# Kernel tuning notes

Measured on AMD Instinct MI355X. Metric: run time of the kernel, lower is better.

Reference implementation:

```python
import jax, jax.numpy as jnp
import numpy as np

IGNORE = -100000.0


def setup_inputs() -> dict:
    key = jax.random.key(0)
    ks = jax.random.split(key, 5)
    b, s, d_model = 4, 2048, 2048
    n_q, n_kv, d_head = 32, 8, 64
    std = 0.02
    return {
        "normalized_resid_pre": jax.random.normal(ks[0], (b, s, d_model), jnp.float32),
        "W_Q": jax.random.normal(ks[1], (n_q, d_model, d_head), jnp.float32) * std,
        "W_K": jax.random.normal(ks[2], (n_kv, d_model, d_head), jnp.float32) * std,
        "W_V": jax.random.normal(ks[3], (n_kv, d_model, d_head), jnp.float32) * std,
        "W_O": jax.random.normal(ks[4], (n_kv, d_head, d_model), jnp.float32) * std,
    }


def reference(normalized_resid_pre, W_Q, W_K, W_V, W_O):
    x = normalized_resid_pre
    b, s, _ = x.shape
    n_kv, d_head = W_K.shape[0], W_K.shape[2]
    n_q = W_Q.shape[0]
    g = n_q // n_kv

    q = jnp.einsum("bpd,hdk->bphk", x, W_Q)  # [b,s,n_q,d_head]
    k = jnp.einsum("bpd,ndk->bpnk", x, W_K)  # [b,s,n_kv,d_head]
    v = jnp.einsum("bpd,ndk->bpnk", x, W_V)  # [b,s,n_kv,d_head]

    # rearrange: head axis splits as (n_kv_heads, g_size), then moved to [b,s,g,n_kv,d_head]
    gq = q.reshape(b, s, n_kv, g, d_head).transpose(0, 1, 3, 2, 4)

    # NOTE: faithful to source — g axis is SUMMED in this einsum
    scores = jnp.einsum("bqgnh,bknh->bnqk", gq, k) / jnp.sqrt(jnp.float32(d_head))

    causal = jnp.triu(jnp.ones((s, s), dtype=bool), k=1)  # True above diagonal
    scores = jnp.where(causal, IGNORE, scores)
    pattern = jax.nn.softmax(scores, axis=-1)  # [b,n_kv,q,k]

    z = jnp.einsum("bknh,bnqk->bqnh", v, pattern)  # [b,s,n_kv,d_head]
    attn_out = jnp.einsum("bqnh,nhd->bqd", z, W_O)  # [b,s,d_model]
    return attn_out
```

## Files before the change

### kernel.cpp

```cpp
#include <hip/hip_runtime.h>

typedef __attribute__((ext_vector_type(8))) _Float16 half8;
typedef __attribute__((ext_vector_type(4))) float f32x4;

#define BATCH  4
#define SLEN   2048
#define DMODEL 2048
#define NKV    8
#define GRP    4
#define DH     64
#define QKV    1536
#define KVDIM  512
#define MROWS  (BATCH * SLEN)

__device__ __forceinline__ unsigned short f2h(float f) {
    union { _Float16 h; unsigned short u; } cv;
    cv.h = (_Float16)f;
    return cv.u;
}

__device__ __forceinline__ void gl16(const void* g, void* l) {
    __builtin_amdgcn_global_load_lds(
        (const __attribute__((address_space(1))) void*)g,
        (__attribute__((address_space(3))) void*)l, 16, 0, 0);
}

typedef __attribute__((ext_vector_type(4))) short short4v;
union U64S4 { unsigned long long u; short4v s; };

__global__ __launch_bounds__(256) void k_pack(const float* __restrict__ wq,
                                              const float* __restrict__ wk,
                                              const float* __restrict__ wv,
                                              float* __restrict__ wcat) {
    int i = blockIdx.x * 256 + threadIdx.x;
    if (i >= DMODEL * QKV) return;
    int d = i / QKV, c = i - d * QKV;
    int mat = c >> 9, rem = c & 511;
    int n = rem >> 6, h = rem & 63;
    float val;
    if (mat == 0) {
        val = 0.0f;
#pragma unroll
        for (int g = 0; g < GRP; ++g)
            val += wq[((size_t)(n * GRP + g) * DMODEL + d) * DH + h];
    } else if (mat == 1) {
        val = wk[((size_t)n * DMODEL + d) * DH + h];
    } else {
        val = wv[((size_t)n * DMODEL + d) * DH + h];
    }
    wcat[(size_t)d * QKV + c] = val;
}

__global__ __launch_bounds__(256) void k_transconv_h(const float* __restrict__ in,
                                                     unsigned short* __restrict__ outT,
                                                     int R, int C) {
    __shared__ float T[64][65];
    const int r0 = blockIdx.x * 64, c0 = blockIdx.y * 64;
    const int tr = threadIdx.x >> 6, tc = threadIdx.x & 63;
#pragma unroll
    for (int i = 0; i < 16; ++i)
        T[tr + i * 4][tc] = in[(size_t)(r0 + tr + i * 4) * C + c0 + tc];
    __syncthreads();
    const int rr = tc;
#pragma unroll
    for (int i = 0; i < 16; ++i) {
        int cc = tr + i * 4;
        outT[(size_t)(c0 + cc) * R + r0 + rr] = f2h(T[rr][cc]);
    }
}

__global__ __launch_bounds__(256) void k_convh(const float* __restrict__ in,
                                               unsigned short* __restrict__ out,
                                               int n4) {
    int i = blockIdx.x * 256 + threadIdx.x;
    if (i >= n4) return;
    float4 v = ((const float4*)in)[i];
    ushort4 o;
    o.x = f2h(v.x); o.y = f2h(v.y); o.z = f2h(v.z); o.w = f2h(v.w);
    ((ushort4*)out)[i] = o;
}

__device__ __forceinline__ void stage_tile64(const unsigned short* __restrict__ src,
                                             unsigned short* lds, int t, int K, int k0) {
#pragma unroll
    for (int j = 0; j < 4; ++j) {
        int slot = j * 256 + t;
        int row = slot >> 3, blk = slot & 7;
        int c = blk ^ (row & 7);
        gl16(src + (size_t)row * K + k0 + c * 8, lds + slot * 8);
    }
}

#define GEMMF16_MAIN(Ag, Bg, K_)                                              \
    const int t = threadIdx.x;                                                \
    const size_t m0 = (size_t)blockIdx.x * 128, n0 = (size_t)blockIdx.y * 128;\
    const int w = t >> 6, l = t & 63;                                         \
    const int wm = (w >> 1) * 64, wn = (w & 1) * 64;                          \
    const int r = l & 15, q = l >> 4;                                         \
    f32x4 acc[4][4] = {};                                                     \
    const int K = (K_);                                                       \
    const int NT = K / 64;                                                    \
    stage_tile64(Ag + m0 * K, A2[0], t, K, 0);                                \
    stage_tile64(Bg + n0 * K, B2[0], t, K, 0);                                \
    asm volatile("s_waitcnt vmcnt(0)" ::: "memory");                          \
    __builtin_amdgcn_s_barrier();                                             \
    int cur = 0;                                                              \
    for (int kt = 0; kt < NT; ++kt) {                                         \
        if (kt + 1 < NT) {                                                    \
            stage_tile64(Ag + m0 * K, A2[cur ^ 1], t, K, (kt + 1) * 64);      \
            stage_tile64(Bg + n0 * K, B2[cur ^ 1], t, K, (kt + 1) * 64);      \
        }                                                                     \
        const unsigned short* Ac = A2[cur];                                   \
        const unsigned short* Bc = B2[cur];                                   \
        half8 af[4][2], bf[4][2];                                             \
        _Pragma("unroll") for (int i = 0; i < 4; ++i)                         \
            _Pragma("unroll") for (int ks = 0; ks < 2; ++ks) {                \
                int ra = wm + i * 16 + r;                                     \
                af[i][ks] = *(const half8*)&Ac[ra * 64 +                      \
                    ((((ks << 2) | q) ^ (ra & 7)) << 3)];                     \
                int rb = wn + i * 16 + r;                                     \
                bf[i][ks] = *(const half8*)&Bc[rb * 64 +                      \
                    ((((ks << 2) | q) ^ (rb & 7)) << 3)];                     \
            }                                                                 \
        __builtin_amdgcn_s_setprio(1);                                        \
        _Pragma("unroll") for (int i = 0; i < 4; ++i)                         \
            _Pragma("unroll") for (int j = 0; j < 4; ++j) {                   \
                acc[i][j] = __builtin_amdgcn_mfma_f32_16x16x32_f16(           \
                    af[i][0], bf[j][0], acc[i][j], 0, 0, 0);                  \
                acc[i][j] = __builtin_amdgcn_mfma_f32_16x16x32_f16(           \
                    af[i][1], bf[j][1], acc[i][j], 0, 0, 0);                  \
            }                                                                 \
        __builtin_amdgcn_s_setprio(0);                                        \
        asm volatile("s_waitcnt vmcnt(0)" ::: "memory");                      \
        __builtin_amdgcn_s_barrier();                                         \
        cur ^= 1;                                                             \
    }

__global__ __launch_bounds__(256) void k_gemm_qkv(
        const unsigned short* __restrict__ Ag, const unsigned short* __restrict__ Bg,
        unsigned short* __restrict__ qk, unsigned short* __restrict__ vT) {
    __shared__ unsigned short A2[2][128 * 64];
    __shared__ unsigned short B2[2][128 * 64];

    GEMMF16_MAIN(Ag, Bg, DMODEL)

    if (n0 < 1024) {
#pragma unroll
        for (int i = 0; i < 4; ++i)
#pragma unroll
            for (int j = 0; j < 4; ++j) {
                int col = (int)n0 + wn + j * 16 + r;
                size_t rowb = m0 + wm + i * 16 + q * 4;
#pragma unroll
                for (int e = 0; e < 4; ++e)
                    qk[(rowb + e) * 1024 + col] = f2h(acc[i][j][e]);
            }
    } else {
#pragma unroll
        for (int i = 0; i < 4; ++i)
#pragma unroll
            for (int j = 0; j < 4; ++j) {
                int d = (int)n0 - 1024 + wn + j * 16 + r;
                size_t rowb = m0 + wm + i * 16 + q * 4;
                ushort4 pk;
                pk.x = f2h(acc[i][j][0]); pk.y = f2h(acc[i][j][1]);
                pk.z = f2h(acc[i][j][2]); pk.w = f2h(acc[i][j][3]);
                *(ushort4*)&vT[(size_t)d * MROWS + rowb] = pk;
            }
    }
}

__global__ __launch_bounds__(256) void k_gemm_out(
        const unsigned short* __restrict__ Ag, const unsigned short* __restrict__ Bg,
        float* __restrict__ C) {
    __shared__ unsigned short A2[2][128 * 64];
    __shared__ unsigned short B2[2][128 * 64];

    GEMMF16_MAIN(Ag, Bg, KVDIM)

#pragma unroll
    for (int i = 0; i < 4; ++i)
#pragma unroll
        for (int j = 0; j < 4; ++j) {
            int col = (int)n0 + wn + j * 16 + r;
            size_t rowb = m0 + wm + i * 16 + q * 4;
#pragma unroll
            for (int e = 0; e < 4; ++e)
                C[(rowb + e) * DMODEL + col] = acc[i][j][e];
        }
}

__global__ __launch_bounds__(256) void k_attn_mfma(
        const unsigned short* __restrict__ qk, const unsigned short* __restrict__ vT,
        unsigned short* __restrict__ zh) {
    __shared__ unsigned short Ks[2][128 * 64];
    __shared__ unsigned short Vs[2][64 * 128];
    __shared__ unsigned short Pt[4 * 128 * 16];

    const int t  = threadIdx.x;
    const int w  = t >> 6, l = t & 63;
    const int p  = blockIdx.x;
    const int n  = blockIdx.y, b = blockIdx.z;
    const int r  = l & 15, g = l >> 4;
    const int wq0 = w * 16;

#define STAGE_KV(buf, kr0)                                                    \
    _Pragma("unroll") for (int j2 = 0; j2 < 4; ++j2) {                        \
        int s2 = j2 * 256 + t;                                                \
        int rK = s2 >> 3, cK = (s2 & 7) ^ (rK & 7);                           \
        gl16(qk + ((kr0) + rK) * 1024 + 512 + n * 64 + cK * 8,                \
             &Ks[buf][s2 * 8]);                                               \
        int rV = s2 >> 4, cV = (s2 & 15) ^ (rV & 15);                         \
        gl16(vT + (size_t)(n * 64 + rV) * MROWS + (kr0) + cV * 8,             \
             &Vs[buf][s2 * 8]);                                               \
    }

#pragma unroll 1
    for (int seg = 0; seg < 2; ++seg) {
        const int qt = seg ? p : (31 - p);
        const int nkt = (qt + 2) >> 1;
        const size_t qrow0 = (size_t)(b * SLEN + qt * 64);

        half8 qh[2];
#pragma unroll
        for (int ks = 0; ks < 2; ++ks) {
            size_t off = (qrow0 + wq0 + r) * 1024 + n * 64 + ks * 32 + g * 8;
            qh[ks] = *(const half8*)(qk + off);
#pragma unroll
            for (int e2 = 0; e2 < 8; ++e2) qh[ks][e2] = qh[ks][e2] * (_Float16)0.125f;
        }

        STAGE_KV(0, (size_t)(b * SLEN))
        asm volatile("s_waitcnt vmcnt(0)" ::: "memory");
        __builtin_amdgcn_s_barrier();

        float m_[4], lsum[4];
#pragma unroll
        for (int e = 0; e < 4; ++e) { m_[e] = -3.0e38f; lsum[e] = 0.0f; }
        f32x4 accz[4] = {};

        for (int kt = 0; kt < nkt; ++kt) {
            const int cur = kt & 1;
            if (kt + 1 < nkt) {
                STAGE_KV(cur ^ 1, (size_t)(b * SLEN + (kt + 1) * 128))
            }
            const unsigned short* Ksc = Ks[cur];
            const unsigned short* Vsc = Vs[cur];

            f32x4 s[8] = {};
#pragma unroll
            for (int ct = 0; ct < 8; ++ct)
#pragma unroll
                for (int ks = 0; ks < 2; ++ks) {
                    int row = ct * 16 + r;
                    int off = row * 128 + (((ks * 4 + g) ^ (row & 7)) << 4);
                    half8 kh8 = *(const half8*)((char*)Ksc + off);
                    s[ct] = __builtin_amdgcn_mfma_f32_16x16x32_f16(qh[ks], kh8, s[ct], 0, 0, 0);
                }

            if (kt == nkt - 1) {
#pragma unroll
                for (int ct = 0; ct < 8; ++ct)
#pragma unroll
                    for (int e = 0; e < 4; ++e)
                        if ((kt * 128 + ct * 16 + r) > (qt * 64 + wq0 + g * 4 + e))
                            s[ct][e] = -100000.0f;
            }

            float al[4], nm[4];
#pragma unroll
            for (int e = 0; e < 4; ++e) {
                float pm = fmaxf(fmaxf(fmaxf(s[0][e], s[1][e]), fmaxf(s[2][e], s[3][e])),
                                 fmaxf(fmaxf(s[4][e], s[5][e]), fmaxf(s[6][e], s[7][e])));
                pm = fmaxf(pm, __shfl_xor(pm, 1));
                pm = fmaxf(pm, __shfl_xor(pm, 2));
                pm = fmaxf(pm, __shfl_xor(pm, 4));
                pm = fmaxf(pm, __shfl_xor(pm, 8));
                nm[e] = fmaxf(m_[e], pm);
                al[e] = __expf(m_[e] - nm[e]);
                m_[e] = nm[e];
            }
            {
                int src = (r >> 2) << 4;
                float a0 = __shfl(al[0], src), a1 = __shfl(al[1], src);
                float a2 = __shfl(al[2], src), a3 = __shfl(al[3], src);
                float ax = (r & 1) ? a1 : a0, ay = (r & 1) ? a3 : a2;
                float aq = (r & 2) ? ay : ax;
#pragma unroll
                for (int dt = 0; dt < 4; ++dt) {
                    accz[dt][0] *= aq; accz[dt][1] *= aq;
                    accz[dt][2] *= aq; accz[dt][3] *= aq;
                }
            }

            float ps[4] = {};
#pragma unroll
            for (int ct = 0; ct < 8; ++ct) {
                float p0 = __expf(s[ct][0] - m_[0]);
                float p1 = __expf(s[ct][1] - m_[1]);
                float p2 = __expf(s[ct][2] - m_[2]);
                float p3 = __expf(s[ct][3] - m_[3]);
                ps[0] += p0; ps[1] += p1; ps[2] += p2; ps[3] += p3;
                short4v pk = { (short)f2h(p0), (short)f2h(p1),
                               (short)f2h(p2), (short)f2h(p3) };
                int kv = ct * 16 + r;
                int phys = (kv >> 5) * 32 + (((kv >> 2) & 1) << 4)
                         + (((kv >> 3) & 3) << 2) + (kv & 3);
                *(short4v*)((char*)Pt + w * 4096 + phys * 32 + g * 8) = pk;
            }

#pragma unroll
            for (int e = 0; e < 4; ++e) {
                float rs = ps[e];
                rs += __shfl_xor(rs, 1); rs += __shfl_xor(rs, 2);
                rs += __shfl_xor(rs, 4); rs += __shfl_xor(rs, 8);
                lsum[e] = lsum[e] * al[e] + rs;
            }

            asm volatile("s_waitcnt lgkmcnt(0)" ::: "memory");
            __builtin_amdgcn_sched_barrier(0);
#pragma unroll
            for (int ks = 0; ks < 4; ++ks) {
                unsigned base = (unsigned)(size_t)((char*)Pt + w * 4096 + ks * 1024) + l * 8;
                U64S4 t1, t2;
                asm volatile("ds_read_b64_tr_b16 %0, %1" : "=v"(t1.u) : "v"(base) : "memory");
                asm volatile("ds_read_b64_tr_b16 %0, %1" : "=v"(t2.u) : "v"(base + 512) : "memory");
                asm volatile("s_waitcnt lgkmcnt(0)" ::: "memory");
                __builtin_amdgcn_sched_barrier(0);
                short4v pa = t1.s, pb = t2.s;
                union { short s[8]; half8 h; } pf;
                pf.s[0] = pa[0]; pf.s[1] = pa[1]; pf.s[2] = pa[2]; pf.s[3] = pa[3];
                pf.s[4] = pb[0]; pf.s[5] = pb[1]; pf.s[6] = pb[2]; pf.s[7] = pb[3];
#pragma unroll
                for (int dt = 0; dt < 4; ++dt) {
                    int d = dt * 16 + r;
                    int off = d * 256 + (((ks * 4 + g) ^ (d & 15)) << 4);
                    half8 vfrag = *(const half8*)((char*)Vsc + off);
                    accz[dt] = __builtin_amdgcn_mfma_f32_16x16x32_f16(vfrag, pf.h, accz[dt], 0, 0, 0);
                }
            }

            asm volatile("s_waitcnt vmcnt(0)" ::: "memory");
            __builtin_amdgcn_s_barrier();
        }

        int src = (r >> 2) << 4;
        float l0 = __shfl(lsum[0], src), l1 = __shfl(lsum[1], src);
        float l2 = __shfl(lsum[2], src), l3 = __shfl(lsum[3], src);
        float lx = (r & 1) ? l1 : l0, ly = (r & 1) ? l3 : l2;
        float inv = 1.0f / ((r & 2) ? ly : lx);
#pragma unroll
        for (int dt = 0; dt < 4; ++dt) {
            ushort4 h4;
#pragma unroll
            for (int e = 0; e < 4; ++e)
                ((unsigned short*)&h4)[e] = f2h(accz[dt][e] * inv);
            size_t off = (qrow0 + wq0 + r) * 512 + n * 64 + dt * 16 + g * 4;
            *(ushort4*)(zh + off) = h4;
        }
    }
#undef STAGE_KV
}

extern "C" void kernel_launch(void* const* d_in, const int* in_sizes, int n_in,
                              void* d_out, int out_size, void* d_ws, size_t ws_size,
                              hipStream_t stream) {
    const float* x  = (const float*)d_in[0];
    const float* wq = (const float*)d_in[1];
    const float* wk = (const float*)d_in[2];
    const float* wv = (const float*)d_in[3];
    const float* wo = (const float*)d_in[4];
    float* out = (float*)d_out;

    char* w = (char*)d_ws;
    unsigned short* xh  = (unsigned short*)(w);
    unsigned short* zh  = (unsigned short*)(w);
    unsigned short* qk  = (unsigned short*)(w + 33554432);
    unsigned short* vT  = (unsigned short*)(w + 50331648);
    unsigned short* wcatT = (unsigned short*)(w + 58720256);
    unsigned short* woT = (unsigned short*)(w + 65011712);
    float*          wcat = (float*)(w + 67108864);

    k_pack<<<dim3((DMODEL * QKV + 255) / 256), 256, 0, stream>>>(wq, wk, wv, wcat);
    k_transconv_h<<<dim3(32, 24), 256, 0, stream>>>(wcat, wcatT, DMODEL, QKV);
    k_transconv_h<<<dim3(8, 32), 256, 0, stream>>>(wo, woT, KVDIM, DMODEL);
    k_convh<<<dim3(16384), 256, 0, stream>>>(x, xh, MROWS * DMODEL / 4);
    k_gemm_qkv<<<dim3(64, 12), 256, 0, stream>>>(xh, wcatT, qk, vT);
    k_attn_mfma<<<dim3(16, NKV, BATCH), 256, 0, stream>>>(qk, vT, zh);
    k_gemm_out<<<dim3(64, 16), 256, 0, stream>>>(zh, woT, out);
}
```

Measured before the change: 201.4 us.

## Fuse weight pack with transpose-convert and widen QKV GEMM tile to 192 columns

```diff
diff --git a/kernel.cpp b/kernel.cpp
--- a/kernel.cpp
+++ b/kernel.cpp
@@ -28,27 +28,38 @@
 typedef __attribute__((ext_vector_type(4))) short short4v;
 union U64S4 { unsigned long long u; short4v s; };
 
-__global__ __launch_bounds__(256) void k_pack(const float* __restrict__ wq,
-                                              const float* __restrict__ wk,
-                                              const float* __restrict__ wv,
-                                              float* __restrict__ wcat) {
-    int i = blockIdx.x * 256 + threadIdx.x;
-    if (i >= DMODEL * QKV) return;
-    int d = i / QKV, c = i - d * QKV;
-    int mat = c >> 9, rem = c & 511;
-    int n = rem >> 6, h = rem & 63;
-    float val;
-    if (mat == 0) {
-        val = 0.0f;
-#pragma unroll
-        for (int g = 0; g < GRP; ++g)
-            val += wq[((size_t)(n * GRP + g) * DMODEL + d) * DH + h];
-    } else if (mat == 1) {
-        val = wk[((size_t)n * DMODEL + d) * DH + h];
-    } else {
-        val = wv[((size_t)n * DMODEL + d) * DH + h];
-    }
-    wcat[(size_t)d * QKV + c] = val;
+__global__ __launch_bounds__(256) void k_packT(const float* __restrict__ wq,
+                                               const float* __restrict__ wk,
+                                               const float* __restrict__ wv,
+                                               unsigned short* __restrict__ outT) {
+    __shared__ float T[64][65];
+    const int d0 = blockIdx.x * 64;
+    const int ct = blockIdx.y;
+    const int mat = ct >> 3, n = ct & 7;
+    const int tr = threadIdx.x >> 6, tc = threadIdx.x & 63;
+#pragma unroll
+    for (int i = 0; i < 16; ++i) {
+        int row = tr + i * 4;
+        float v;
+        if (mat == 0) {
+            v = 0.0f;
+#pragma unroll
+            for (int g = 0; g < GRP; ++g)
+                v += wq[((size_t)(n * GRP + g) * DMODEL + d0 + row) * DH + tc];
+        } else if (mat == 1) {
+            v = wk[((size_t)n * DMODEL + d0 + row) * DH + tc];
+        } else {
+            v = wv[((size_t)n * DMODEL + d0 + row) * DH + tc];
+        }
+        T[row][tc] = v;
+    }
+    __syncthreads();
+    const int rr = tc;
+#pragma unroll
+    for (int i = 0; i < 16; ++i) {
+        int cc = tr + i * 4;
+        outT[(size_t)(mat * 512 + n * 64 + cc) * DMODEL + d0 + rr] = f2h(T[rr][cc]);
+    }
 }
 
 __global__ __launch_bounds__(256) void k_transconv_h(const float* __restrict__ in,
@@ -80,10 +91,12 @@
     ((ushort4*)out)[i] = o;
 }
 
-__device__ __forceinline__ void stage_tile64(const unsigned short* __restrict__ src,
-                                             unsigned short* lds, int t, int K, int k0) {
-#pragma unroll
-    for (int j = 0; j < 4; ++j) {
+__device__ __forceinline__ void stage_rows(const unsigned short* __restrict__ src,
+                                           unsigned short* lds, int t, int K,
+                                           int k0, int nslots4) {
+#pragma unroll
+    for (int j = 0; j < 8; ++j) {
+        if (j >= nslots4) break;
         int slot = j * 256 + t;
         int row = slot >> 3, blk = slot & 7;
         int c = blk ^ (row & 7);
@@ -91,83 +104,80 @@
     }
 }
 
-#define GEMMF16_MAIN(Ag, Bg, K_)                                              \
-    const int t = threadIdx.x;                                                \
-    const size_t m0 = (size_t)blockIdx.x * 128, n0 = (size_t)blockIdx.y * 128;\
-    const int w = t >> 6, l = t & 63;                                         \
-    const int wm = (w >> 1) * 64, wn = (w & 1) * 64;                          \
-    const int r = l & 15, q = l >> 4;                                         \
-    f32x4 acc[4][4] = {};                                                     \
-    const int K = (K_);                                                       \
-    const int NT = K / 64;                                                    \
-    stage_tile64(Ag + m0 * K, A2[0], t, K, 0);                                \
-    stage_tile64(Bg + n0 * K, B2[0], t, K, 0);                                \
-    asm volatile("s_waitcnt vmcnt(0)" ::: "memory");                          \
-    __builtin_amdgcn_s_barrier();                                             \
-    int cur = 0;                                                              \
-    for (int kt = 0; kt < NT; ++kt) {                                         \
-        if (kt + 1 < NT) {                                                    \
-            stage_tile64(Ag + m0 * K, A2[cur ^ 1], t, K, (kt + 1) * 64);      \
-            stage_tile64(Bg + n0 * K, B2[cur ^ 1], t, K, (kt + 1) * 64);      \
-        }                                                                     \
-        const unsigned short* Ac = A2[cur];                                   \
-        const unsigned short* Bc = B2[cur];                                   \
-        half8 af[4][2], bf[4][2];                                             \
-        _Pragma("unroll") for (int i = 0; i < 4; ++i)                         \
-            _Pragma("unroll") for (int ks = 0; ks < 2; ++ks) {                \
-                int ra = wm + i * 16 + r;                                     \
-                af[i][ks] = *(const half8*)&Ac[ra * 64 +                      \
-                    ((((ks << 2) | q) ^ (ra & 7)) << 3)];                     \
-                int rb = wn + i * 16 + r;                                     \
-                bf[i][ks] = *(const half8*)&Bc[rb * 64 +                      \
-                    ((((ks << 2) | q) ^ (rb & 7)) << 3)];                     \
-            }                                                                 \
-        __builtin_amdgcn_s_setprio(1);                                        \
-        _Pragma("unroll") for (int i = 0; i < 4; ++i)                         \
-            _Pragma("unroll") for (int j = 0; j < 4; ++j) {                   \
-                acc[i][j] = __builtin_amdgcn_mfma_f32_16x16x32_f16(           \
-                    af[i][0], bf[j][0], acc[i][j], 0, 0, 0);                  \
-                acc[i][j] = __builtin_amdgcn_mfma_f32_16x16x32_f16(           \
-                    af[i][1], bf[j][1], acc[i][j], 0, 0, 0);                  \
-            }                                                                 \
-        __builtin_amdgcn_s_setprio(0);                                        \
-        asm volatile("s_waitcnt vmcnt(0)" ::: "memory");                      \
-        __builtin_amdgcn_s_barrier();                                         \
-        cur ^= 1;                                                             \
-    }
-
 __global__ __launch_bounds__(256) void k_gemm_qkv(
         const unsigned short* __restrict__ Ag, const unsigned short* __restrict__ Bg,
         unsigned short* __restrict__ qk, unsigned short* __restrict__ vT) {
     __shared__ unsigned short A2[2][128 * 64];
-    __shared__ unsigned short B2[2][128 * 64];
-
-    GEMMF16_MAIN(Ag, Bg, DMODEL)
-
-    if (n0 < 1024) {
+    __shared__ unsigned short B2[2][192 * 64];
+
+    const int t = threadIdx.x;
+    const size_t m0 = (size_t)blockIdx.x * 128, n0 = (size_t)blockIdx.y * 192;
+    const int w = t >> 6, l = t & 63;
+    const int wm = (w >> 1) * 64, wn = (w & 1) * 96;
+    const int r = l & 15, q = l >> 4;
+    f32x4 acc[4][6] = {};
+    const int K = DMODEL;
+    const int NT = K / 64;
+
+    stage_rows(Ag + m0 * K, A2[0], t, K, 0, 4);
+    stage_rows(Bg + n0 * K, B2[0], t, K, 0, 6);
+    asm volatile("s_waitcnt vmcnt(0)" ::: "memory");
+    __builtin_amdgcn_s_barrier();
+    int cur = 0;
+    for (int kt = 0; kt < NT; ++kt) {
+        if (kt + 1 < NT) {
+            stage_rows(Ag + m0 * K, A2[cur ^ 1], t, K, (kt + 1) * 64, 4);
+            stage_rows(Bg + n0 * K, B2[cur ^ 1], t, K, (kt + 1) * 64, 6);
+        }
+        const unsigned short* Ac = A2[cur];
+        const unsigned short* Bc = B2[cur];
+        half8 af[4][2], bf[6][2];
 #pragma unroll
         for (int i = 0; i < 4; ++i)
 #pragma unroll
-            for (int j = 0; j < 4; ++j) {
-                int col = (int)n0 + wn + j * 16 + r;
-                size_t rowb = m0 + wm + i * 16 + q * 4;
+            for (int ks = 0; ks < 2; ++ks) {
+                int ra = wm + i * 16 + r;
+                af[i][ks] = *(const half8*)&Ac[ra * 64 + ((((ks << 2) | q) ^ (ra & 7)) << 3)];
+            }
+#pragma unroll
+        for (int j = 0; j < 6; ++j)
+#pragma unroll
+            for (int ks = 0; ks < 2; ++ks) {
+                int rb = wn + j * 16 + r;
+                bf[j][ks] = *(const half8*)&Bc[rb * 64 + ((((ks << 2) | q) ^ (rb & 7)) << 3)];
+            }
+        __builtin_amdgcn_s_setprio(1);
+#pragma unroll
+        for (int i = 0; i < 4; ++i)
+#pragma unroll
+            for (int j = 0; j < 6; ++j) {
+                acc[i][j] = __builtin_amdgcn_mfma_f32_16x16x32_f16(af[i][0], bf[j][0], acc[i][j], 0, 0, 0);
+                acc[i][j] = __builtin_amdgcn_mfma_f32_16x16x32_f16(af[i][1], bf[j][1], acc[i][j], 0, 0, 0);
+            }
+        __builtin_amdgcn_s_setprio(0);
+        asm volatile("s_waitcnt vmcnt(0)" ::: "memory");
+        __builtin_amdgcn_s_barrier();
+        cur ^= 1;
+    }
+
+#pragma unroll
+    for (int i = 0; i < 4; ++i)
+#pragma unroll
+        for (int j = 0; j < 6; ++j) {
+            int col = (int)n0 + wn + j * 16 + r;
+            size_t rowb = m0 + wm + i * 16 + q * 4;
+            if (col < 1024) {
 #pragma unroll
                 for (int e = 0; e < 4; ++e)
                     qk[(rowb + e) * 1024 + col] = f2h(acc[i][j][e]);
-            }
-    } else {
-#pragma unroll
-        for (int i = 0; i < 4; ++i)
-#pragma unroll
-            for (int j = 0; j < 4; ++j) {
-                int d = (int)n0 - 1024 + wn + j * 16 + r;
-                size_t rowb = m0 + wm + i * 16 + q * 4;
+            } else {
+                int d = col - 1024;
                 ushort4 pk;
                 pk.x = f2h(acc[i][j][0]); pk.y = f2h(acc[i][j][1]);
                 pk.z = f2h(acc[i][j][2]); pk.w = f2h(acc[i][j][3]);
                 *(ushort4*)&vT[(size_t)d * MROWS + rowb] = pk;
             }
-    }
+        }
 }
 
 __global__ __launch_bounds__(256) void k_gemm_out(
@@ -176,7 +186,50 @@
     __shared__ unsigned short A2[2][128 * 64];
     __shared__ unsigned short B2[2][128 * 64];
 
-    GEMMF16_MAIN(Ag, Bg, KVDIM)
+    const int t = threadIdx.x;
+    const size_t m0 = (size_t)blockIdx.x * 128, n0 = (size_t)blockIdx.y * 128;
+    const int w = t >> 6, l = t & 63;
+    const int wm = (w >> 1) * 64, wn = (w & 1) * 64;
+    const int r = l & 15, q = l >> 4;
+    f32x4 acc[4][4] = {};
+    const int K = KVDIM;
+    const int NT = K / 64;
+
+    stage_rows(Ag + m0 * K, A2[0], t, K, 0, 4);
+    stage_rows(Bg + n0 * K, B2[0], t, K, 0, 4);
+    asm volatile("s_waitcnt vmcnt(0)" ::: "memory");
+    __builtin_amdgcn_s_barrier();
+    int cur = 0;
+    for (int kt = 0; kt < NT; ++kt) {
+        if (kt + 1 < NT) {
+            stage_rows(Ag + m0 * K, A2[cur ^ 1], t, K, (kt + 1) * 64, 4);
+            stage_rows(Bg + n0 * K, B2[cur ^ 1], t, K, (kt + 1) * 64, 4);
+        }
+        const unsigned short* Ac = A2[cur];
+        const unsigned short* Bc = B2[cur];
+        half8 af[4][2], bf[4][2];
+#pragma unroll
+        for (int i = 0; i < 4; ++i)
+#pragma unroll
+            for (int ks = 0; ks < 2; ++ks) {
+                int ra = wm + i * 16 + r;
+                af[i][ks] = *(const half8*)&Ac[ra * 64 + ((((ks << 2) | q) ^ (ra & 7)) << 3)];
+                int rb = wn + i * 16 + r;
+                bf[i][ks] = *(const half8*)&Bc[rb * 64 + ((((ks << 2) | q) ^ (rb & 7)) << 3)];
+            }
+        __builtin_amdgcn_s_setprio(1);
+#pragma unroll
+        for (int i = 0; i < 4; ++i)
+#pragma unroll
+            for (int j = 0; j < 4; ++j) {
+                acc[i][j] = __builtin_amdgcn_mfma_f32_16x16x32_f16(af[i][0], bf[j][0], acc[i][j], 0, 0, 0);
+                acc[i][j] = __builtin_amdgcn_mfma_f32_16x16x32_f16(af[i][1], bf[j][1], acc[i][j], 0, 0, 0);
+            }
+        __builtin_amdgcn_s_setprio(0);
+        asm volatile("s_waitcnt vmcnt(0)" ::: "memory");
+        __builtin_amdgcn_s_barrier();
+        cur ^= 1;
+    }
 
 #pragma unroll
     for (int i = 0; i < 4; ++i)
@@ -379,13 +432,11 @@
     unsigned short* vT  = (unsigned short*)(w + 50331648);
     unsigned short* wcatT = (unsigned short*)(w + 58720256);
     unsigned short* woT = (unsigned short*)(w + 65011712);
-    float*          wcat = (float*)(w + 67108864);
-
-    k_pack<<<dim3((DMODEL * QKV + 255) / 256), 256, 0, stream>>>(wq, wk, wv, wcat);
-    k_transconv_h<<<dim3(32, 24), 256, 0, stream>>>(wcat, wcatT, DMODEL, QKV);
+
+    k_packT<<<dim3(32, 24), 256, 0, stream>>>(wq, wk, wv, wcatT);
     k_transconv_h<<<dim3(8, 32), 256, 0, stream>>>(wo, woT, KVDIM, DMODEL);
     k_convh<<<dim3(16384), 256, 0, stream>>>(x, xh, MROWS * DMODEL / 4);
-    k_gemm_qkv<<<dim3(64, 12), 256, 0, stream>>>(xh, wcatT, qk, vT);
+    k_gemm_qkv<<<dim3(64, 8), 256, 0, stream>>>(xh, wcatT, qk, vT);
     k_attn_mfma<<<dim3(16, NKV, BATCH), 256, 0, stream>>>(qk, vT, zh);
     k_gemm_out<<<dim3(64, 16), 256, 0, stream>>>(zh, woT, out);
 }
```

Measured after the change: 187.8 us. -6.8%, faster.
